# Kernel optimization log

Hardware: AMD Instinct MI355X
Metric: run time of the kernel (lower is better)

## Reference

```python
import jax, jax.numpy as jnp
import numpy as np

B, C, CI, H, W = 8, 256, 64, 64, 64  # batch, in_channels, inter_channels, spatial


def conv1x1(x, w, b):
    # x: [B,C,H,W], w: [O,C] (1x1 kernel), b: [O]
    return jnp.einsum('bchw,oc->bohw', x, w) + b[None, :, None, None]


def setup_inputs() -> dict:
    key = jax.random.key(0)
    ks = jax.random.split(key, 9)
    s_in = 1.0 / np.sqrt(C)
    s_ci = 1.0 / np.sqrt(CI)
    return {
        'x': jax.random.normal(ks[0], (B, C, H, W), dtype=jnp.float32),
        'g_w': jax.random.uniform(ks[1], (CI, C), jnp.float32, -s_in, s_in),
        'g_b': jax.random.uniform(ks[2], (CI,), jnp.float32, -s_in, s_in),
        'theta_w': jax.random.uniform(ks[3], (CI, C), jnp.float32, -s_in, s_in),
        'theta_b': jax.random.uniform(ks[4], (CI,), jnp.float32, -s_in, s_in),
        'phi_w': jax.random.uniform(ks[5], (CI, C), jnp.float32, -s_in, s_in),
        'phi_b': jax.random.uniform(ks[6], (CI,), jnp.float32, -s_in, s_in),
        'w_w': jax.random.uniform(ks[7], (C, CI), jnp.float32, -s_ci, s_ci),
        'w_b': jax.random.uniform(ks[8], (C,), jnp.float32, -s_ci, s_ci),
    }


def reference(x, g_w, g_b, theta_w, theta_b, phi_w, phi_b, w_w, w_b):
    b, c, h, w = x.shape
    n = h * w
    # 1x1 conv projections, flattened over spatial positions -> [B, N, CI]
    g_x = conv1x1(x, g_w, g_b).reshape(b, CI, n).transpose(0, 2, 1)
    theta_x = conv1x1(x, theta_w, theta_b).reshape(b, CI, n).transpose(0, 2, 1)
    phi_x = conv1x1(x, phi_w, phi_b).reshape(b, CI, n)  # [B, CI, N]
    # Full non-scaled attention over spatial positions
    f = jnp.einsum('bnc,bcm->bnm', theta_x, phi_x)       # [B, N, N]
    f_div_c = jax.nn.softmax(f, axis=-1)
    y = jnp.einsum('bnm,bmc->bnc', f_div_c, g_x)         # [B, N, CI]
    y = y.transpose(0, 2, 1).reshape(b, CI, h, w)
    w_y = conv1x1(y, w_w, w_b)                            # [B, C, H, W]
    return w_y + x
```

## Files before the change

### kernel.cpp

```cpp
#include <hip/hip_runtime.h>
#include <hip/hip_bf16.h>

#define B_  8
#define C_  256
#define CI_ 64
#define N_  4096
#define KSPLIT 4
#define KTILES (N_ / 64 / KSPLIT)

typedef short short8  __attribute__((ext_vector_type(8)));
typedef short sh4     __attribute__((ext_vector_type(4)));
typedef float floatx4 __attribute__((ext_vector_type(4)));

#define LOG2E 1.4426950408889634f

__device__ __forceinline__ unsigned short f2bf(float f) {
    unsigned u = __builtin_bit_cast(unsigned, f);
    u += 0x7FFFu + ((u >> 16) & 1u);
    return (unsigned short)(u >> 16);
}
__device__ __forceinline__ float bf2f(unsigned short h) {
    unsigned u = ((unsigned)h) << 16;
    return __builtin_bit_cast(float, u);
}

__device__ __forceinline__ unsigned pk2(float a, float b) {
#if __has_builtin(__builtin_amdgcn_cvt_pk_bf16_f32)
    auto r = __builtin_amdgcn_cvt_pk_bf16_f32(a, b);
    return __builtin_bit_cast(unsigned, r);
#else
    return (unsigned)f2bf(a) | ((unsigned)f2bf(b) << 16);
#endif
}

__device__ __forceinline__ floatx4 mfma32(short8 a, short8 b, floatx4 c) {
    return __builtin_amdgcn_mfma_f32_16x16x32_bf16(a, b, c, 0, 0, 0);
}
__device__ __forceinline__ floatx4 mfma16(sh4 a, sh4 b, floatx4 c) {
#if __has_builtin(__builtin_amdgcn_mfma_f32_16x16x16bf16_1k)
    return __builtin_amdgcn_mfma_f32_16x16x16bf16_1k(a, b, c, 0, 0, 0);
#else
    floatx4 d;
    asm("v_mfma_f32_16x16x16_bf16 %0, %1, %2, %3" : "=v"(d) : "v"(a), "v"(b), "v"(c));
    return d;
#endif
}

__global__ __launch_bounds__(512, 4) void proj_kernel(
    const float* __restrict__ x,
    const float* __restrict__ wg, const float* __restrict__ bg,
    const float* __restrict__ wt, const float* __restrict__ bt,
    const float* __restrict__ wp, const float* __restrict__ bp,
    unsigned short* __restrict__ gws,
    unsigned short* __restrict__ tws,
    unsigned short* __restrict__ pws)
{
    constexpr int WS = 40;
    constexpr int GS = 72;
    __shared__ __align__(16) unsigned short wsl[2][192 * WS];
    __shared__ __align__(16) unsigned short gt[64 * GS];

    const int t    = threadIdx.x;
    const int lane = t & 63;
    const int w    = t >> 6;
    const int nf   = w >> 1;
    const int oh   = w & 1;
    const int l15  = lane & 15;
    const int quad = lane >> 4;
    const int n0   = blockIdx.x * 64;
    const int b    = blockIdx.y;

    floatx4 acc[6];
#pragma unroll
    for (int i = 0; i < 6; ++i) { floatx4 z = {0.f, 0.f, 0.f, 0.f}; acc[i] = z; }

    const int nA = n0 + nf * 16 + l15;
    const float* xbase = x + (size_t)b * C_ * N_ + nA;

    float xv[64];
#pragma unroll
    for (int kk = 0; kk < 8; ++kk)
#pragma unroll
        for (int j = 0; j < 8; ++j)
            xv[kk * 8 + j] = xbase[(size_t)(kk * 32 + quad * 8 + j) * N_];

#pragma unroll
    for (int it = 0; it < 3; ++it) {
        int u = t + it * 512;
        int row = u >> 3, c4 = u & 7;
        const float* src = (row < 64)  ? (wg + row * C_)
                         : (row < 128) ? (wt + (row - 64) * C_)
                                       : (wp + (row - 128) * C_);
        const float sc = (row >= 64 && row < 128) ? LOG2E : 1.0f;
        float4 v = *(const float4*)(src + c4 * 4);
        uint2 uu = { pk2(v.x * sc, v.y * sc), pk2(v.z * sc, v.w * sc) };
        *(uint2*)&wsl[0][row * WS + c4 * 4] = uu;
    }
    __syncthreads();

    for (int kk = 0; kk < 8; ++kk) {
        uint4 au = { pk2(xv[kk * 8 + 0], xv[kk * 8 + 1]),
                     pk2(xv[kk * 8 + 2], xv[kk * 8 + 3]),
                     pk2(xv[kk * 8 + 4], xv[kk * 8 + 5]),
                     pk2(xv[kk * 8 + 6], xv[kk * 8 + 7]) };
        short8 af = __builtin_bit_cast(short8, au);

        if (kk < 7) {
#pragma unroll
            for (int it = 0; it < 3; ++it) {
                int u = t + it * 512;
                int row = u >> 3, c4 = u & 7;
                const float* src = (row < 64)  ? (wg + row * C_)
                                 : (row < 128) ? (wt + (row - 64) * C_)
                                               : (wp + (row - 128) * C_);
                const float sc = (row >= 64 && row < 128) ? LOG2E : 1.0f;
                float4 v = *(const float4*)(src + (kk + 1) * 32 + c4 * 4);
                uint2 uu = { pk2(v.x * sc, v.y * sc), pk2(v.z * sc, v.w * sc) };
                *(uint2*)&wsl[(kk + 1) & 1][row * WS + c4 * 4] = uu;
            }
        }

#pragma unroll
        for (int oti = 0; oti < 6; ++oti) {
            const int ot = oh * 6 + oti;
            short8 bf = *(const short8*)&wsl[kk & 1][(ot * 16 + l15) * WS + quad * 8];
            acc[oti] = mfma32(af, bf, acc[oti]);
        }
        __syncthreads();
    }

#pragma unroll
    for (int oti = 0; oti < 6; ++oti) {
        const int ot = oh * 6 + oti;
        const int oc = ot * 16 + l15;
        const float bias = (ot < 4) ? bg[oc]
                         : (ot < 8) ? bt[oc - 64] * LOG2E
                                    : bp[oc - 128];
        if (ot < 4) {
#pragma unroll
            for (int r = 0; r < 4; ++r)
                gt[oc * GS + nf * 16 + quad * 4 + r] = f2bf(acc[oti][r] + bias);
        } else {
            unsigned short* dst = (ot < 8) ? tws : pws;
            const int ci = (ot < 8) ? (oc - 64) : (oc - 128);
#pragma unroll
            for (int r = 0; r < 4; ++r) {
                int n = n0 + nf * 16 + quad * 4 + r;
                dst[((size_t)b * N_ + n) * CI_ + ci] = f2bf(acc[oti][r] + bias);
            }
        }
    }
    __syncthreads();
    {
        int ci = t >> 3, n8 = t & 7;
        uint4 v = *(const uint4*)&gt[ci * GS + n8 * 8];
        *(uint4*)(gws + ((size_t)b * CI_ + ci) * N_ + n0 + n8 * 8) = v;
    }
}

__global__ __launch_bounds__(256, 4) void attn_kernel(
    const unsigned short* __restrict__ gws,
    const unsigned short* __restrict__ tws,
    const unsigned short* __restrict__ pws,
    unsigned short* __restrict__ Opart,
    float* __restrict__ lpart)
{
    constexpr int LDW = 72;
    __shared__ __align__(16) unsigned short Vs[2][64 * LDW];

    const int t    = threadIdx.x;
    const int lane = t & 63;
    const int w    = t >> 6;
    const int l15  = lane & 15;
    const int quad = lane >> 4;
    const int b    = blockIdx.x;
    const int q0   = blockIdx.y * 128;
    const int sp   = blockIdx.z;

    const int srow = t >> 3;
    const int sc8  = t & 7;

    const unsigned short* kslice = pws + ((size_t)b * N_ + sp * (N_ / KSPLIT)) * CI_;
    const unsigned short* vbase  =
        gws + ((size_t)b * CI_ + srow) * N_ + sp * (N_ / KSPLIT) + sc8 * 8;

    short8 qf[2][2];
#pragma unroll
    for (int qg = 0; qg < 2; ++qg) {
        const unsigned short* qrow =
            tws + ((size_t)b * N_ + q0 + w * 32 + qg * 16 + l15) * CI_;
        qf[qg][0] = *(const short8*)(qrow + quad * 8);
        qf[qg][1] = *(const short8*)(qrow + 32 + quad * 8);
    }

    {
        uint4 v0 = *(const uint4*)(vbase);
        uint4 v1 = *(const uint4*)(vbase + 32 * N_);
        *(uint4*)&Vs[0][srow * LDW + sc8 * 8]        = v0;
        *(uint4*)&Vs[0][(srow + 32) * LDW + sc8 * 8] = v1;
    }
    __syncthreads();

    sh4 ones4;
#pragma unroll
    for (int j = 0; j < 4; ++j) ones4[j] = (short)0x3F80;

    floatx4 Oacc[2][4], lacc[2];
    { floatx4 z = {0.f, 0.f, 0.f, 0.f};
      lacc[0] = z; lacc[1] = z;
#pragma unroll
      for (int qg = 0; qg < 2; ++qg)
#pragma unroll
          for (int f = 0; f < 4; ++f) Oacc[qg][f] = z; }

    for (int j = 0; j < KTILES; ++j) {
        const int p  = j & 1;
        const int jn = (j + 1) & (KTILES - 1);

        uint4 pv0 = *(const uint4*)(vbase + jn * 64);
        uint4 pv1 = *(const uint4*)(vbase + 32 * N_ + jn * 64);

        const unsigned short* kt = kslice + (size_t)j * 64 * CI_;
        short8 ka[4][2];
#pragma unroll
        for (int f = 0; f < 4; ++f) {
            ka[f][0] = *(const short8*)(kt + (f * 16 + l15) * CI_ + quad * 8);
            ka[f][1] = *(const short8*)(kt + (f * 16 + l15) * CI_ + 32 + quad * 8);
        }

#pragma unroll
        for (int f = 0; f < 4; ++f) {
            sh4 pfr[2];
#pragma unroll
            for (int qg = 0; qg < 2; ++qg) {
                floatx4 s = {0.f, 0.f, 0.f, 0.f};
                s = mfma32(ka[f][0], qf[qg][0], s);
                s = mfma32(ka[f][1], qf[qg][1], s);
                uint2 uu = { pk2(__builtin_amdgcn_exp2f(s[0]),
                                 __builtin_amdgcn_exp2f(s[1])),
                             pk2(__builtin_amdgcn_exp2f(s[2]),
                                 __builtin_amdgcn_exp2f(s[3])) };
                pfr[qg] = __builtin_bit_cast(sh4, uu);
                lacc[qg] = mfma16(pfr[qg], ones4, lacc[qg]);
            }
#pragma unroll
            for (int fc = 0; fc < 4; ++fc) {
                sh4 vb = *(const sh4*)&Vs[p][(fc * 16 + l15) * LDW + f * 16 + quad * 4];
#pragma unroll
                for (int qg = 0; qg < 2; ++qg)
                    Oacc[qg][fc] = mfma16(pfr[qg], vb, Oacc[qg][fc]);
            }
        }

        *(uint4*)&Vs[1 - p][srow * LDW + sc8 * 8]        = pv0;
        *(uint4*)&Vs[1 - p][(srow + 32) * LDW + sc8 * 8] = pv1;

        __syncthreads();
    }

#pragma unroll
    for (int qg = 0; qg < 2; ++qg) {
#pragma unroll
        for (int r = 0; r < 4; ++r) {
            int row = q0 + w * 32 + qg * 16 + quad * 4 + r;
            size_t obase = ((size_t)(sp * B_ + b) * N_ + row) * CI_;
#pragma unroll
            for (int fc = 0; fc < 4; ++fc)
                Opart[obase + fc * 16 + l15] = f2bf(Oacc[qg][fc][r]);
            if (l15 == 0)
                lpart[(size_t)(sp * B_ + b) * N_ + row] = lacc[qg][r];
        }
    }
}

__global__ __launch_bounds__(256, 4) void out_kernel(
    const unsigned short* __restrict__ Opart,
    const float* __restrict__ lpart,
    const float* __restrict__ ww,
    const float* __restrict__ wb,
    const float* __restrict__ x,
    float* __restrict__ out)
{
    constexpr int WS = 72;
    constexpr int TS = 66;
    __shared__ __align__(16) char smem[128 * TS * 4];
    unsigned short* wws = (unsigned short*)smem;
    float*          T   = (float*)smem;

    const int t    = threadIdx.x;
    const int lane = t & 63;
    const int w    = t >> 6;
    const int l15  = lane & 15;
    const int quad = lane >> 4;
    const int n0   = blockIdx.x * 64;
    const int b    = blockIdx.y;
    const int ch   = blockIdx.z;

#pragma unroll
    for (int it = 0; it < 8; ++it) {
        int u = t + it * 256;
        int row = u >> 4, c4 = u & 15;
        float4 v = *(const float4*)(ww + (ch * 128 + row) * CI_ + c4 * 4);
        uint2 uu = { pk2(v.x, v.y), pk2(v.z, v.w) };
        *(uint2*)&wws[row * WS + c4 * 4] = uu;
    }
    __syncthreads();

    floatx4 acc[8];
#pragma unroll
    for (int ot = 0; ot < 8; ++ot) { floatx4 z = {0.f, 0.f, 0.f, 0.f}; acc[ot] = z; }

    const int nB = n0 + w * 16 + l15;
    float lsum = 0.f;
#pragma unroll
    for (int sp = 0; sp < KSPLIT; ++sp)
        lsum += lpart[(size_t)(sp * B_ + b) * N_ + nB];
    const float inv = 1.f / lsum;

#pragma unroll
    for (int ks = 0; ks < 2; ++ks) {
        float ysum[8] = {0.f, 0.f, 0.f, 0.f, 0.f, 0.f, 0.f, 0.f};
#pragma unroll
        for (int sp = 0; sp < KSPLIT; ++sp) {
            short8 ov = *(const short8*)(Opart +
                ((size_t)(sp * B_ + b) * N_ + nB) * CI_ + ks * 32 + quad * 8);
#pragma unroll
            for (int e = 0; e < 8; ++e)
                ysum[e] += bf2f((unsigned short)ov[e]);
        }
        uint4 bu = { pk2(ysum[0] * inv, ysum[1] * inv),
                     pk2(ysum[2] * inv, ysum[3] * inv),
                     pk2(ysum[4] * inv, ysum[5] * inv),
                     pk2(ysum[6] * inv, ysum[7] * inv) };
        short8 bfrag = __builtin_bit_cast(short8, bu);
#pragma unroll
        for (int ot = 0; ot < 8; ++ot) {
            short8 afrag = *(const short8*)&wws[(ot * 16 + l15) * WS + ks * 32 + quad * 8];
            acc[ot] = mfma32(afrag, bfrag, acc[ot]);
        }
    }
    __syncthreads();

#pragma unroll
    for (int ot = 0; ot < 8; ++ot) {
#pragma unroll
        for (int r = 0; r < 4; ++r) {
            int cr = ot * 16 + quad * 4 + r;
            T[cr * TS + w * 16 + l15] = acc[ot][r] + wb[ch * 128 + cr];
        }
    }
    __syncthreads();

    const int c0 = t >> 4;
    const int nq = t & 15;
#pragma unroll
    for (int i = 0; i < 8; ++i) {
        int cr = c0 + 16 * i;
        float4 tv = *(const float4*)&T[cr * TS + nq * 4];
        size_t idx = ((size_t)b * C_ + ch * 128 + cr) * N_ + n0 + nq * 4;
        float4 xv = *(const float4*)(x + idx);
        float4 ov = { tv.x + xv.x, tv.y + xv.y, tv.z + xv.z, tv.w + xv.w };
        *(float4*)(out + idx) = ov;
    }
}

extern "C" void kernel_launch(void* const* d_in, const int* in_sizes, int n_in,
                              void* d_out, int out_size, void* d_ws, size_t ws_size,
                              hipStream_t stream) {
    const float* x  = (const float*)d_in[0];
    const float* gw = (const float*)d_in[1];
    const float* gb = (const float*)d_in[2];
    const float* tw = (const float*)d_in[3];
    const float* tb = (const float*)d_in[4];
    const float* pw = (const float*)d_in[5];
    const float* pb = (const float*)d_in[6];
    const float* ww = (const float*)d_in[7];
    const float* wb = (const float*)d_in[8];
    float* out = (float*)d_out;

    char* ws = (char*)d_ws;
    unsigned short* gws   = (unsigned short*)(ws);
    unsigned short* tws   = (unsigned short*)(ws + (4  << 20));
    unsigned short* pws   = (unsigned short*)(ws + (8  << 20));
    unsigned short* Opart = (unsigned short*)(ws + (12 << 20));
    float*          lpart = (float*)        (ws + (28 << 20));

    proj_kernel<<<dim3(64, 8), 512, 0, stream>>>(x, gw, gb, tw, tb, pw, pb, gws, tws, pws);
    attn_kernel<<<dim3(8, 32, KSPLIT), 256, 0, stream>>>(gws, tws, pws, Opart, lpart);
    out_kernel<<<dim3(64, 8, 2), 256, 0, stream>>>(Opart, lpart, ww, wb, x, out);
}
```

Before: 188.9 us.

## Halve attention query tile per block to raise occupancy

Each wave now processes one 16-row query group instead of two, so each block covers 64 queries and the grid doubles along the query axis. Launch bounds rise to 8 blocks per CU, cutting accumulator registers per thread. This trades reuse of the K fragments and V shared-memory tiles across two query groups for more resident waves to hide latency. K/V load traffic per query doubles.

```diff
diff --git a/kernel.cpp b/kernel.cpp
--- a/kernel.cpp
+++ b/kernel.cpp
@@ -158,7 +158,7 @@
     }
 }
 
-__global__ __launch_bounds__(256, 4) void attn_kernel(
+__global__ __launch_bounds__(256, 8) void attn_kernel(
     const unsigned short* __restrict__ gws,
     const unsigned short* __restrict__ tws,
     const unsigned short* __restrict__ pws,
@@ -174,7 +174,7 @@
     const int l15  = lane & 15;
     const int quad = lane >> 4;
     const int b    = blockIdx.x;
-    const int q0   = blockIdx.y * 128;
+    const int q0   = blockIdx.y * 64;
     const int sp   = blockIdx.z;
 
     const int srow = t >> 3;
@@ -184,13 +184,12 @@
     const unsigned short* vbase  =
         gws + ((size_t)b * CI_ + srow) * N_ + sp * (N_ / KSPLIT) + sc8 * 8;
 
-    short8 qf[2][2];
-#pragma unroll
-    for (int qg = 0; qg < 2; ++qg) {
+    short8 qf0, qf1;
+    {
         const unsigned short* qrow =
-            tws + ((size_t)b * N_ + q0 + w * 32 + qg * 16 + l15) * CI_;
-        qf[qg][0] = *(const short8*)(qrow + quad * 8);
-        qf[qg][1] = *(const short8*)(qrow + 32 + quad * 8);
+            tws + ((size_t)b * N_ + q0 + w * 16 + l15) * CI_;
+        qf0 = *(const short8*)(qrow + quad * 8);
+        qf1 = *(const short8*)(qrow + 32 + quad * 8);
     }
 
     {
@@ -203,15 +202,13 @@
 
     sh4 ones4;
 #pragma unroll
-    for (int j = 0; j < 4; ++j) ones4[j] = (short)0x3F80;
-
-    floatx4 Oacc[2][4], lacc[2];
+    for (int j4 = 0; j4 < 4; ++j4) ones4[j4] = (short)0x3F80;
+
+    floatx4 Oacc[4], lacc;
     { floatx4 z = {0.f, 0.f, 0.f, 0.f};
-      lacc[0] = z; lacc[1] = z;
-#pragma unroll
-      for (int qg = 0; qg < 2; ++qg)
-#pragma unroll
-          for (int f = 0; f < 4; ++f) Oacc[qg][f] = z; }
+      lacc = z;
+#pragma unroll
+      for (int fc = 0; fc < 4; ++fc) Oacc[fc] = z; }
 
     for (int j = 0; j < KTILES; ++j) {
         const int p  = j & 1;
@@ -230,25 +227,19 @@
 
 #pragma unroll
         for (int f = 0; f < 4; ++f) {
-            sh4 pfr[2];
-#pragma unroll
-            for (int qg = 0; qg < 2; ++qg) {
-                floatx4 s = {0.f, 0.f, 0.f, 0.f};
-                s = mfma32(ka[f][0], qf[qg][0], s);
-                s = mfma32(ka[f][1], qf[qg][1], s);
-                uint2 uu = { pk2(__builtin_amdgcn_exp2f(s[0]),
-                                 __builtin_amdgcn_exp2f(s[1])),
-                             pk2(__builtin_amdgcn_exp2f(s[2]),
-                                 __builtin_amdgcn_exp2f(s[3])) };
-                pfr[qg] = __builtin_bit_cast(sh4, uu);
-                lacc[qg] = mfma16(pfr[qg], ones4, lacc[qg]);
-            }
+            floatx4 s = {0.f, 0.f, 0.f, 0.f};
+            s = mfma32(ka[f][0], qf0, s);
+            s = mfma32(ka[f][1], qf1, s);
+            uint2 uu = { pk2(__builtin_amdgcn_exp2f(s[0]),
+                             __builtin_amdgcn_exp2f(s[1])),
+                         pk2(__builtin_amdgcn_exp2f(s[2]),
+                             __builtin_amdgcn_exp2f(s[3])) };
+            sh4 pfr = __builtin_bit_cast(sh4, uu);
+            lacc = mfma16(pfr, ones4, lacc);
 #pragma unroll
             for (int fc = 0; fc < 4; ++fc) {
                 sh4 vb = *(const sh4*)&Vs[p][(fc * 16 + l15) * LDW + f * 16 + quad * 4];
-#pragma unroll
-                for (int qg = 0; qg < 2; ++qg)
-                    Oacc[qg][fc] = mfma16(pfr[qg], vb, Oacc[qg][fc]);
+                Oacc[fc] = mfma16(pfr, vb, Oacc[fc]);
             }
         }
 
@@ -259,17 +250,14 @@
     }
 
 #pragma unroll
-    for (int qg = 0; qg < 2; ++qg) {
-#pragma unroll
-        for (int r = 0; r < 4; ++r) {
-            int row = q0 + w * 32 + qg * 16 + quad * 4 + r;
-            size_t obase = ((size_t)(sp * B_ + b) * N_ + row) * CI_;
-#pragma unroll
-            for (int fc = 0; fc < 4; ++fc)
-                Opart[obase + fc * 16 + l15] = f2bf(Oacc[qg][fc][r]);
-            if (l15 == 0)
-                lpart[(size_t)(sp * B_ + b) * N_ + row] = lacc[qg][r];
-        }
+    for (int r = 0; r < 4; ++r) {
+        int row = q0 + w * 16 + quad * 4 + r;
+        size_t obase = ((size_t)(sp * B_ + b) * N_ + row) * CI_;
+#pragma unroll
+        for (int fc = 0; fc < 4; ++fc)
+            Opart[obase + fc * 16 + l15] = f2bf(Oacc[fc][r]);
+        if (l15 == 0)
+            lpart[(size_t)(sp * B_ + b) * N_ + row] = lacc[r];
     }
 }
 
@@ -386,6 +374,6 @@
     float*          lpart = (float*)        (ws + (28 << 20));
 
     proj_kernel<<<dim3(64, 8), 512, 0, stream>>>(x, gw, gb, tw, tb, pw, pb, gws, tws, pws);
-    attn_kernel<<<dim3(8, 32, KSPLIT), 256, 0, stream>>>(gws, tws, pws, Opart, lpart);
+    attn_kernel<<<dim3(8, 64, KSPLIT), 256, 0, stream>>>(gws, tws, pws, Opart, lpart);
     out_kernel<<<dim3(64, 8, 2), 256, 0, stream>>>(Opart, lpart, ww, wb, x, out);
 }
```

Result: slower. 244.7 us (+29.5%).
